# Kernel optimization log

Measured on AMD Instinct MI355X. Metric: run time of the kernel, lower is better.

Reference implementation:

```python
import jax, jax.numpy as jnp
import numpy as np

N_NODES = 50000


def setup_inputs() -> dict:
    key = jax.random.key(0)
    ks = jax.random.split(key, 6)
    nfeat, nhid, hops, nedges = 256, 64, 4, 800000
    x = jax.random.normal(ks[0], (N_NODES, nfeat), dtype=jnp.float32)
    W = jax.random.normal(ks[1], (hops, nfeat, nhid), dtype=jnp.float32) / np.sqrt(nfeat)
    b = jax.random.normal(ks[2], (hops, nhid), dtype=jnp.float32) * 0.01
    adj_rows = jax.random.randint(ks[3], (hops, nedges), 0, N_NODES, dtype=jnp.int32)
    adj_cols = jax.random.randint(ks[4], (hops, nedges), 0, N_NODES, dtype=jnp.int32)
    # normalize-ish positive edge weights, as in a GCN-normalized adjacency
    adj_vals = jax.random.uniform(ks[5], (hops, nedges), dtype=jnp.float32) / 16.0
    return {"x": x, "W": W, "b": b, "adj_rows": adj_rows,
            "adj_cols": adj_cols, "adj_vals": adj_vals}


def reference(x, W, b, adj_rows, adj_cols, adj_vals):
    # SIGN forward (eval mode: dropout = identity).
    # For each hop i: h = x @ W[i] + b[i]; out_i = spmm(adj_i, h)
    # spmm in COO form: out[r] = sum_{e: rows[e]==r} vals[e] * h[cols[e]]
    n = x.shape[0]
    hops = W.shape[0]
    outs = []
    for i in range(hops):  # small fixed hop count (layers+1)
        h = x @ W[i] + b[i]                      # [N, nhid] dense GEMM
        msgs = adj_vals[i][:, None] * h[adj_cols[i]]  # [E, nhid] gather
        outs.append(jax.ops.segment_sum(msgs, adj_rows[i], num_segments=n))
    return jax.nn.elu(jnp.concatenate(outs, axis=1))  # [N, hops*nhid]
```

## Files before the change

### kernel.cpp

```cpp
#include <hip/hip_runtime.h>
#include <hip/hip_bf16.h>
#include <math.h>

#define N_NODES 50000
#define NFEAT 256
#define NHID 64
#define HOPS 4
#define NEDGES 800000
#define NBINS (HOPS * N_NODES)

#define BROWS 256
#define NBUCK 196
#define NBK_ALL (HOPS * NBUCK)
#define CHUNK 8192
#define NCHUNK ((NEDGES + CHUNK - 1) / CHUNK)
#define FS_CAP 8192

#define GM 64
#define LDP 40
#define NGBLK ((N_NODES + GM - 1) / GM)

typedef short bf16x8 __attribute__((ext_vector_type(8)));
typedef float f32x4 __attribute__((ext_vector_type(4)));

static __device__ __forceinline__ unsigned short f2bf(float f) {
    __hip_bfloat16 h = __float2bfloat16(f);
    return *reinterpret_cast<unsigned short*>(&h);
}

__global__ __launch_bounds__(256) void castx_kernel(const float* __restrict__ x,
                                                    unsigned short* __restrict__ Xbf) {
    const int i = blockIdx.x * 256 + threadIdx.x;
    const size_t base = (size_t)i * 8;
    if (base < (size_t)N_NODES * NFEAT) {
        const float4 a = *(const float4*)&x[base];
        const float4 c = *(const float4*)&x[base + 4];
        unsigned short o[8] = {f2bf(a.x), f2bf(a.y), f2bf(a.z), f2bf(a.w),
                               f2bf(c.x), f2bf(c.y), f2bf(c.z), f2bf(c.w)};
        *(bf16x8*)&Xbf[base] = *(const bf16x8*)o;
    }
}

__global__ __launch_bounds__(256) void castw_kernel(const float* __restrict__ W,
                                                    unsigned short* __restrict__ Wt) {
    const int idx = blockIdx.x * 256 + threadIdx.x;
    if (idx < HOPS * NFEAT * NHID) {
        const int hop = idx >> 14;
        const int k = (idx >> 6) & 255;
        const int c = idx & 63;
        Wt[((size_t)(hop * 64 + c)) * NFEAT + k] = f2bf(W[idx]);
    }
}

__global__ __launch_bounds__(256) void gemm_bf_kernel(const unsigned short* __restrict__ Xbf,
                                                      const unsigned short* __restrict__ Wt,
                                                      const float* __restrict__ b,
                                                      __hip_bfloat16* __restrict__ H) {
    __shared__ unsigned short A_lds[GM * LDP];
    __shared__ unsigned short B_lds[256 * LDP];

    const int t = threadIdx.x;
    const int lane = t & 63;
    const int w = t >> 6;
    const int quad = lane >> 4;
    const int m16 = lane & 15;
    const int row0 = blockIdx.x * GM;

    f32x4 acc[4][4];
#pragma unroll
    for (int mt = 0; mt < 4; ++mt)
#pragma unroll
        for (int nt = 0; nt < 4; ++nt) acc[mt][nt] = (f32x4){0.f, 0.f, 0.f, 0.f};

    for (int ks = 0; ks < 8; ++ks) {
        const int k0 = ks * 32;
        {
            const int r = t >> 2;
            const int kq = (t & 3) * 8;
            bf16x8 v = {0, 0, 0, 0, 0, 0, 0, 0};
            if (row0 + r < N_NODES)
                v = *(const bf16x8*)&Xbf[(size_t)(row0 + r) * NFEAT + k0 + kq];
            *(bf16x8*)&A_lds[r * LDP + kq] = v;
        }
#pragma unroll
        for (int q = 0; q < 4; ++q) {
            const int kq = q * 8;
            const bf16x8 v = *(const bf16x8*)&Wt[(size_t)t * NFEAT + k0 + kq];
            *(bf16x8*)&B_lds[t * LDP + kq] = v;
        }
        __syncthreads();

        bf16x8 af[4], bf[4];
#pragma unroll
        for (int mt = 0; mt < 4; ++mt)
            af[mt] = *(const bf16x8*)&A_lds[(mt * 16 + m16) * LDP + quad * 8];
#pragma unroll
        for (int nt = 0; nt < 4; ++nt)
            bf[nt] = *(const bf16x8*)&B_lds[(w * 64 + nt * 16 + m16) * LDP + quad * 8];
#pragma unroll
        for (int mt = 0; mt < 4; ++mt)
#pragma unroll
            for (int nt = 0; nt < 4; ++nt)
                acc[mt][nt] = __builtin_amdgcn_mfma_f32_16x16x32_bf16(
                    af[mt], bf[nt], acc[mt][nt], 0, 0, 0);
        __syncthreads();
    }

#pragma unroll
    for (int nt = 0; nt < 4; ++nt) {
        const int col = w * 64 + nt * 16 + m16;
        const float bias = b[col];
#pragma unroll
        for (int mt = 0; mt < 4; ++mt) {
#pragma unroll
            for (int r = 0; r < 4; ++r) {
                const int row = row0 + mt * 16 + quad * 4 + r;
                if (row < N_NODES)
                    H[(size_t)row * 256 + col] = __float2bfloat16(acc[mt][nt][r] + bias);
            }
        }
    }
}

__global__ __launch_bounds__(256) void gemm_mfma_kernel(const float* __restrict__ x,
                                                        const float* __restrict__ W,
                                                        const float* __restrict__ b,
                                                        __hip_bfloat16* __restrict__ H) {
    __shared__ unsigned short A_lds[GM * LDP];
    __shared__ unsigned short B_lds[256 * LDP];

    const int t = threadIdx.x;
    const int lane = t & 63;
    const int w = t >> 6;
    const int quad = lane >> 4;
    const int m16 = lane & 15;
    const int row0 = blockIdx.x * GM;

    f32x4 acc[4][4];
#pragma unroll
    for (int mt = 0; mt < 4; ++mt)
#pragma unroll
        for (int nt = 0; nt < 4; ++nt) acc[mt][nt] = (f32x4){0.f, 0.f, 0.f, 0.f};

    for (int ks = 0; ks < 8; ++ks) {
        const int k0 = ks * 32;
#pragma unroll
        for (int it = 0; it < 2; ++it) {
            const int i = t + it * 256;
            const int r = i >> 3;
            const int kq = (i & 7) * 4;
            float4 v = make_float4(0.f, 0.f, 0.f, 0.f);
            if (row0 + r < N_NODES)
                v = *(const float4*)&x[(size_t)(row0 + r) * NFEAT + k0 + kq];
            unsigned short* d = &A_lds[r * LDP + kq];
            d[0] = f2bf(v.x); d[1] = f2bf(v.y); d[2] = f2bf(v.z); d[3] = f2bf(v.w);
        }
#pragma unroll
        for (int it = 0; it < 8; ++it) {
            const int i = t + it * 256;
            const int n4 = i & 63;
            const int kk = i >> 6;
            const int hop = n4 >> 4;
            const int j = (n4 & 15) * 4;
            const float4 v = *(const float4*)&W[(size_t)hop * (NFEAT * NHID)
                                                + (size_t)(k0 + kk) * NHID + j];
            B_lds[(n4 * 4 + 0) * LDP + kk] = f2bf(v.x);
            B_lds[(n4 * 4 + 1) * LDP + kk] = f2bf(v.y);
            B_lds[(n4 * 4 + 2) * LDP + kk] = f2bf(v.z);
            B_lds[(n4 * 4 + 3) * LDP + kk] = f2bf(v.w);
        }
        __syncthreads();

        bf16x8 af[4], bf[4];
#pragma unroll
        for (int mt = 0; mt < 4; ++mt)
            af[mt] = *(const bf16x8*)&A_lds[(mt * 16 + m16) * LDP + quad * 8];
#pragma unroll
        for (int nt = 0; nt < 4; ++nt)
            bf[nt] = *(const bf16x8*)&B_lds[(w * 64 + nt * 16 + m16) * LDP + quad * 8];
#pragma unroll
        for (int mt = 0; mt < 4; ++mt)
#pragma unroll
            for (int nt = 0; nt < 4; ++nt)
                acc[mt][nt] = __builtin_amdgcn_mfma_f32_16x16x32_bf16(
                    af[mt], bf[nt], acc[mt][nt], 0, 0, 0);
        __syncthreads();
    }

#pragma unroll
    for (int nt = 0; nt < 4; ++nt) {
        const int col = w * 64 + nt * 16 + m16;
        const float bias = b[col];
#pragma unroll
        for (int mt = 0; mt < 4; ++mt) {
#pragma unroll
            for (int r = 0; r < 4; ++r) {
                const int row = row0 + mt * 16 + quad * 4 + r;
                if (row < N_NODES)
                    H[(size_t)row * 256 + col] = __float2bfloat16(acc[mt][nt][r] + bias);
            }
        }
    }
}

__global__ __launch_bounds__(256) void bhist_kernel(const int* __restrict__ rows,
                                                    int* __restrict__ bucket_cnt) {
    __shared__ int h[NBUCK];
    const int t = threadIdx.x;
    for (int i = t; i < NBUCK; i += 256) h[i] = 0;
    __syncthreads();
    const int hop = blockIdx.y;
    const int e0 = blockIdx.x * CHUNK;
    const int n = min(CHUNK, NEDGES - e0);
    const size_t base = (size_t)hop * NEDGES + e0;
    for (int i = t; i < n; i += 256) {
        atomicAdd(&h[rows[base + i] >> 8], 1);
    }
    __syncthreads();
    for (int i = t; i < NBUCK; i += 256) {
        if (h[i]) atomicAdd(&bucket_cnt[hop * NBUCK + i], h[i]);
    }
}

__global__ __launch_bounds__(256) void bscan_kernel(const int* __restrict__ cnt,
                                                    int* __restrict__ start,
                                                    int* __restrict__ cursor,
                                                    int* __restrict__ offsets) {
    __shared__ int s[256];
    const int t = threadIdx.x;
    int v[4];
    int tsum = 0;
#pragma unroll
    for (int i = 0; i < 4; ++i) {
        const int idx = t * 4 + i;
        v[i] = (idx < NBK_ALL) ? cnt[idx] : 0;
        tsum += v[i];
    }
    s[t] = tsum;
    __syncthreads();
    for (int off = 1; off < 256; off <<= 1) {
        const int a = (t >= off) ? s[t - off] : 0;
        __syncthreads();
        s[t] += a;
        __syncthreads();
    }
    int run = s[t] - tsum;
#pragma unroll
    for (int i = 0; i < 4; ++i) {
        const int idx = t * 4 + i;
        if (idx < NBK_ALL) {
            start[idx] = run;
            cursor[idx] = run;
            run += v[i];
        }
    }
    if (t == 255) {
        start[NBK_ALL] = run;
        offsets[NBINS] = run;
    }
}

__global__ __launch_bounds__(256) void partition_kernel(const int* __restrict__ rows,
                                                        const int* __restrict__ cols,
                                                        const float* __restrict__ vals,
                                                        int* __restrict__ cursor,
                                                        int2* __restrict__ partbuf) {
    __shared__ int2 pay[CHUNK];
    __shared__ int h[NBUCK], excl[NBUCK], gbase[NBUCK], lcur[NBUCK];
    __shared__ int s[256];
    const int t = threadIdx.x;
    const int hop = blockIdx.y;
    const int e0 = blockIdx.x * CHUNK;
    const int n = min(CHUNK, NEDGES - e0);
    const size_t base = (size_t)hop * NEDGES + e0;

    for (int i = t; i < NBUCK; i += 256) h[i] = 0;
    __syncthreads();

    int myrow[CHUNK / 256];
#pragma unroll
    for (int j = 0; j < CHUNK / 256; ++j) {
        const int i = t + j * 256;
        if (i < n) {
            const int r = rows[base + i];
            myrow[j] = r;
            atomicAdd(&h[r >> 8], 1);
        }
    }
    __syncthreads();

    const int hv = (t < NBUCK) ? h[t] : 0;
    s[t] = hv;
    __syncthreads();
    for (int off = 1; off < 256; off <<= 1) {
        const int a = (t >= off) ? s[t - off] : 0;
        __syncthreads();
        s[t] += a;
        __syncthreads();
    }
    if (t < NBUCK) {
        const int ex = s[t] - hv;
        excl[t] = ex;
        lcur[t] = ex;
        gbase[t] = hv ? atomicAdd(&cursor[hop * NBUCK + t], hv) : 0;
    }
    __syncthreads();

#pragma unroll
    for (int j = 0; j < CHUNK / 256; ++j) {
        const int i = t + j * 256;
        if (i < n) {
            const int r = myrow[j];
            const int c = cols[base + i];
            const float v = vals[base + i];
            const int pos = atomicAdd(&lcur[r >> 8], 1);
            pay[pos] = make_int2((r << 16) | c, __float_as_int(v));
        }
    }
    __syncthreads();

    for (int i = t; i < n; i += 256) {
        const int2 p = pay[i];
        const int bk = ((unsigned)p.x) >> 24;
        partbuf[gbase[bk] + (i - excl[bk])] = p;
    }
}

__global__ __launch_bounds__(256) void fsort_kernel(const int* __restrict__ start,
                                                    int2* __restrict__ partbuf,
                                                    int* __restrict__ offsets) {
    __shared__ int2 pay[FS_CAP];
    __shared__ int h[BROWS], excl[BROWS], cur[BROWS];
    __shared__ int s[256];
    const int t = threadIdx.x;
    const int hop = blockIdx.y;
    const int bucket = blockIdx.x;
    const int g = hop * NBUCK + bucket;
    const int s0 = start[g];
    const int n = min(start[g + 1] - s0, FS_CAP);

    h[t] = 0;
    __syncthreads();

    for (int i = t; i < n; i += 256) {
        const int2 p = partbuf[s0 + i];
        pay[i] = p;
        atomicAdd(&h[((unsigned)p.x >> 16) & 255], 1);
    }
    __syncthreads();

    const int hv = h[t];
    s[t] = hv;
    __syncthreads();
    for (int off = 1; off < 256; off <<= 1) {
        const int a = (t >= off) ? s[t - off] : 0;
        __syncthreads();
        s[t] += a;
        __syncthreads();
    }
    const int ex = s[t] - hv;
    excl[t] = ex;
    cur[t] = 0;
    const int row = bucket * BROWS + t;
    if (row < N_NODES) offsets[hop * N_NODES + row] = s0 + ex;
    __syncthreads();

    for (int i = t; i < n; i += 256) {
        const int2 p = pay[i];
        const int rl = ((unsigned)p.x >> 16) & 255;
        const int pos = s0 + excl[rl] + atomicAdd(&cur[rl], 1);
        partbuf[pos] = make_int2(p.x & 0xFFFF, p.y);
    }
}

__global__ __launch_bounds__(256) void csr_gather_kernel(const __hip_bfloat16* __restrict__ H,
                                                         const int* __restrict__ offsets,
                                                         const int2* __restrict__ epk,
                                                         float* __restrict__ out) {
    const int t = threadIdx.x;
    const int f = t & 63;
    const int w = t >> 6;
    const int hop = blockIdx.y;
    const int row0w = blockIdx.x * 64 + w * 16;
    if (row0w >= N_NODES) return;
    const int bin0 = hop * N_NODES + row0w;

    int off_l = 0;
    if (f <= 16) off_l = offsets[bin0 + f];

    const unsigned short* Hf = (const unsigned short*)H + hop * 64 + f;
    float* outp = out + (size_t)row0w * 256 + hop * 64 + f;

    for (int r = 0; r < 16; ++r) {
        const int s  = __builtin_amdgcn_readlane(off_l, r);
        const int e2 = __builtin_amdgcn_readlane(off_l, r + 1);
        float acc = 0.f;
        int e = s;
        for (; e + 8 <= e2; e += 8) {
            const int2 m = epk[e + (f & 7)];
            float h8[8];
#pragma unroll
            for (int j = 0; j < 8; ++j) {
                const int col = __builtin_amdgcn_readlane(m.x, j);
                h8[j] = __uint_as_float((unsigned)Hf[(size_t)col << 8] << 16);
            }
#pragma unroll
            for (int j = 0; j < 8; ++j) {
                const float val = __uint_as_float((unsigned)__builtin_amdgcn_readlane(m.y, j));
                acc = fmaf(val, h8[j], acc);
            }
        }
        if (e < e2) {
            const int2 m = epk[e + (f & 7)];
            const int rem = e2 - e;
            for (int j = 0; j < rem; ++j) {
                const int col = __builtin_amdgcn_readlane(m.x, j);
                const float val = __uint_as_float((unsigned)__builtin_amdgcn_readlane(m.y, j));
                acc = fmaf(val, __uint_as_float((unsigned)Hf[(size_t)col << 8] << 16), acc);
            }
        }
        acc = acc > 0.f ? acc : expf(acc) - 1.f;
        outp[(size_t)r * 256] = acc;
    }
}

#define EPW 8
__global__ __launch_bounds__(256) void scatter_kernel(const __hip_bfloat16* __restrict__ H,
                                                      const int* __restrict__ rows,
                                                      const int* __restrict__ cols,
                                                      const float* __restrict__ vals,
                                                      float* __restrict__ out) {
    const int lane = threadIdx.x & 63;
    const int wid = __builtin_amdgcn_readfirstlane(threadIdx.x >> 6);
    const int hop = blockIdx.y;
    const int e0 = (blockIdx.x * 4 + wid) * EPW;
    const int base = hop * NEDGES;
    const int hoff = hop * 64 + lane;
#pragma unroll
    for (int i = 0; i < EPW; ++i) {
        const int e = e0 + i;
        const int r = rows[base + e];
        const int c = cols[base + e];
        const float v = vals[base + e];
        unsafeAtomicAdd(&out[(size_t)r * 256 + hoff],
                        v * __bfloat162float(H[(size_t)c * 256 + hoff]));
    }
}

__global__ __launch_bounds__(256) void elu_kernel(float* __restrict__ out, int n4) {
    const int i = blockIdx.x * 256 + threadIdx.x;
    if (i < n4) {
        float4 v = ((float4*)out)[i];
        v.x = v.x > 0.f ? v.x : expf(v.x) - 1.f;
        v.y = v.y > 0.f ? v.y : expf(v.y) - 1.f;
        v.z = v.z > 0.f ? v.z : expf(v.z) - 1.f;
        v.w = v.w > 0.f ? v.w : expf(v.w) - 1.f;
        ((float4*)out)[i] = v;
    }
}

extern "C" void kernel_launch(void* const* d_in, const int* in_sizes, int n_in,
                              void* d_out, int out_size, void* d_ws, size_t ws_size,
                              hipStream_t stream) {
    const float* x        = (const float*)d_in[0];
    const float* W        = (const float*)d_in[1];
    const float* b        = (const float*)d_in[2];
    const int*   adj_rows = (const int*)d_in[3];
    const int*   adj_cols = (const int*)d_in[4];
    const float* adj_vals = (const float*)d_in[5];
    float* out = (float*)d_out;

    char* w = (char*)d_ws;
    size_t off = 0;
    __hip_bfloat16* H = (__hip_bfloat16*)(w + off);
    off += (size_t)N_NODES * 256 * 2;
    int2*  partbuf    = (int2*)(w + off);  off += (size_t)HOPS * NEDGES * 8;
    int*   offsets    = (int*)(w + off);   off += (((size_t)(NBINS + 1)) * 4 + 255) & ~255ull;
    int*   bucket_cnt = (int*)(w + off);   off += ((size_t)NBK_ALL * 4 + 255) & ~255ull;
    int*   bstart     = (int*)(w + off);   off += (((size_t)NBK_ALL + 1) * 4 + 255) & ~255ull;
    int*   bcursor    = (int*)(w + off);   off += ((size_t)NBK_ALL * 4 + 255) & ~255ull;
    const bool use_sorted = (ws_size >= off);

    unsigned short* Xbf = (unsigned short*)partbuf;
    unsigned short* Wt  = (unsigned short*)offsets;

    if (use_sorted) {
        castx_kernel<<<(N_NODES * NFEAT / 8 + 255) / 256, 256, 0, stream>>>(x, Xbf);
        castw_kernel<<<(HOPS * NFEAT * NHID + 255) / 256, 256, 0, stream>>>(W, Wt);
        gemm_bf_kernel<<<NGBLK, 256, 0, stream>>>(Xbf, Wt, b, H);

        hipMemsetAsync(bucket_cnt, 0, (size_t)NBK_ALL * 4, stream);
        bhist_kernel<<<dim3(NCHUNK, HOPS), 256, 0, stream>>>(adj_rows, bucket_cnt);
        bscan_kernel<<<1, 256, 0, stream>>>(bucket_cnt, bstart, bcursor, offsets);
        partition_kernel<<<dim3(NCHUNK, HOPS), 256, 0, stream>>>(adj_rows, adj_cols,
                                                                 adj_vals, bcursor, partbuf);
        fsort_kernel<<<dim3(NBUCK, HOPS), 256, 0, stream>>>(bstart, partbuf, offsets);
        csr_gather_kernel<<<dim3((N_NODES + 63) / 64, HOPS), 256, 0, stream>>>(
            H, offsets, partbuf, out);
    } else {
        gemm_mfma_kernel<<<NGBLK, 256, 0, stream>>>(x, W, b, H);
        hipMemsetAsync(d_out, 0, (size_t)out_size * sizeof(float), stream);
        scatter_kernel<<<dim3(NEDGES / (4 * EPW), HOPS), 256, 0, stream>>>(
            H, adj_rows, adj_cols, adj_vals, out);
        elu_kernel<<<(out_size / 4 + 255) / 256, 256, 0, stream>>>(out, out_size / 4);
    }
}
```

Baseline: 361.5 us.

## Shrink sort buckets to 64 rows and stage per-wave edge metadata in LDS

```diff
diff --git a/kernel.cpp b/kernel.cpp
--- a/kernel.cpp
+++ b/kernel.cpp
@@ -9,12 +9,13 @@
 #define NEDGES 800000
 #define NBINS (HOPS * N_NODES)
 
-#define BROWS 256
-#define NBUCK 196
+#define BROWS 64
+#define NBUCK 782
 #define NBK_ALL (HOPS * NBUCK)
-#define CHUNK 8192
+#define CHUNK 4096
 #define NCHUNK ((NEDGES + CHUNK - 1) / CHUNK)
-#define FS_CAP 8192
+#define FS_CAP 2048
+#define MCAP 512
 
 #define GM 64
 #define LDP 40
@@ -214,7 +215,7 @@
     const int n = min(CHUNK, NEDGES - e0);
     const size_t base = (size_t)hop * NEDGES + e0;
     for (int i = t; i < n; i += 256) {
-        atomicAdd(&h[rows[base + i] >> 8], 1);
+        atomicAdd(&h[rows[base + i] >> 6], 1);
     }
     __syncthreads();
     for (int i = t; i < NBUCK; i += 256) {
@@ -222,17 +223,18 @@
     }
 }
 
+#define SCAN_V ((NBK_ALL + 255) / 256)
 __global__ __launch_bounds__(256) void bscan_kernel(const int* __restrict__ cnt,
                                                     int* __restrict__ start,
                                                     int* __restrict__ cursor,
                                                     int* __restrict__ offsets) {
     __shared__ int s[256];
     const int t = threadIdx.x;
-    int v[4];
+    int v[SCAN_V];
     int tsum = 0;
 #pragma unroll
-    for (int i = 0; i < 4; ++i) {
-        const int idx = t * 4 + i;
+    for (int i = 0; i < SCAN_V; ++i) {
+        const int idx = t * SCAN_V + i;
         v[i] = (idx < NBK_ALL) ? cnt[idx] : 0;
         tsum += v[i];
     }
@@ -246,8 +248,8 @@
     }
     int run = s[t] - tsum;
 #pragma unroll
-    for (int i = 0; i < 4; ++i) {
-        const int idx = t * 4 + i;
+    for (int i = 0; i < SCAN_V; ++i) {
+        const int idx = t * SCAN_V + i;
         if (idx < NBK_ALL) {
             start[idx] = run;
             cursor[idx] = run;
@@ -284,13 +286,20 @@
         if (i < n) {
             const int r = rows[base + i];
             myrow[j] = r;
-            atomicAdd(&h[r >> 8], 1);
-        }
-    }
-    __syncthreads();
-
-    const int hv = (t < NBUCK) ? h[t] : 0;
-    s[t] = hv;
+            atomicAdd(&h[r >> 6], 1);
+        }
+    }
+    __syncthreads();
+
+    int pv[4];
+    int tsum = 0;
+#pragma unroll
+    for (int i = 0; i < 4; ++i) {
+        const int idx = t * 4 + i;
+        pv[i] = (idx < NBUCK) ? h[idx] : 0;
+        tsum += pv[i];
+    }
+    s[t] = tsum;
     __syncthreads();
     for (int off = 1; off < 256; off <<= 1) {
         const int a = (t >= off) ? s[t - off] : 0;
@@ -298,11 +307,16 @@
         s[t] += a;
         __syncthreads();
     }
-    if (t < NBUCK) {
-        const int ex = s[t] - hv;
-        excl[t] = ex;
-        lcur[t] = ex;
-        gbase[t] = hv ? atomicAdd(&cursor[hop * NBUCK + t], hv) : 0;
+    int run = s[t] - tsum;
+#pragma unroll
+    for (int i = 0; i < 4; ++i) {
+        const int idx = t * 4 + i;
+        if (idx < NBUCK) {
+            excl[idx] = run;
+            lcur[idx] = run;
+            gbase[idx] = pv[i] ? atomicAdd(&cursor[hop * NBUCK + idx], pv[i]) : 0;
+            run += pv[i];
+        }
     }
     __syncthreads();
 
@@ -313,7 +327,7 @@
             const int r = myrow[j];
             const int c = cols[base + i];
             const float v = vals[base + i];
-            const int pos = atomicAdd(&lcur[r >> 8], 1);
+            const int pos = atomicAdd(&lcur[r >> 6], 1);
             pay[pos] = make_int2((r << 16) | c, __float_as_int(v));
         }
     }
@@ -321,7 +335,7 @@
 
     for (int i = t; i < n; i += 256) {
         const int2 p = pay[i];
-        const int bk = ((unsigned)p.x) >> 24;
+        const int bk = ((unsigned)p.x) >> 22;
         partbuf[gbase[bk] + (i - excl[bk])] = p;
     }
 }
@@ -339,17 +353,17 @@
     const int s0 = start[g];
     const int n = min(start[g + 1] - s0, FS_CAP);
 
-    h[t] = 0;
+    if (t < BROWS) h[t] = 0;
     __syncthreads();
 
     for (int i = t; i < n; i += 256) {
         const int2 p = partbuf[s0 + i];
         pay[i] = p;
-        atomicAdd(&h[((unsigned)p.x >> 16) & 255], 1);
-    }
-    __syncthreads();
-
-    const int hv = h[t];
+        atomicAdd(&h[((unsigned)p.x >> 16) & (BROWS - 1)], 1);
+    }
+    __syncthreads();
+
+    const int hv = (t < BROWS) ? h[t] : 0;
     s[t] = hv;
     __syncthreads();
     for (int off = 1; off < 256; off <<= 1) {
@@ -358,16 +372,18 @@
         s[t] += a;
         __syncthreads();
     }
-    const int ex = s[t] - hv;
-    excl[t] = ex;
-    cur[t] = 0;
-    const int row = bucket * BROWS + t;
-    if (row < N_NODES) offsets[hop * N_NODES + row] = s0 + ex;
+    if (t < BROWS) {
+        const int ex = s[t] - hv;
+        excl[t] = ex;
+        cur[t] = 0;
+        const int row = bucket * BROWS + t;
+        if (row < N_NODES) offsets[hop * N_NODES + row] = s0 + ex;
+    }
     __syncthreads();
 
     for (int i = t; i < n; i += 256) {
         const int2 p = pay[i];
-        const int rl = ((unsigned)p.x >> 16) & 255;
+        const int rl = ((unsigned)p.x >> 16) & (BROWS - 1);
         const int pos = s0 + excl[rl] + atomicAdd(&cur[rl], 1);
         partbuf[pos] = make_int2(p.x & 0xFFFF, p.y);
     }
@@ -377,6 +393,7 @@
                                                          const int* __restrict__ offsets,
                                                          const int2* __restrict__ epk,
                                                          float* __restrict__ out) {
+    __shared__ int2 meta[4][MCAP + 8];
     const int t = threadIdx.x;
     const int f = t & 63;
     const int w = t >> 6;
@@ -387,40 +404,75 @@
 
     int off_l = 0;
     if (f <= 16) off_l = offsets[bin0 + f];
+    const int s0w = __builtin_amdgcn_readlane(off_l, 0);
+    const int s1w = __builtin_amdgcn_readlane(off_l, 16);
+    const int cnt = s1w - s0w;
 
     const unsigned short* Hf = (const unsigned short*)H + hop * 64 + f;
     float* outp = out + (size_t)row0w * 256 + hop * 64 + f;
 
-    for (int r = 0; r < 16; ++r) {
-        const int s  = __builtin_amdgcn_readlane(off_l, r);
-        const int e2 = __builtin_amdgcn_readlane(off_l, r + 1);
-        float acc = 0.f;
-        int e = s;
-        for (; e + 8 <= e2; e += 8) {
-            const int2 m = epk[e + (f & 7)];
-            float h8[8];
-#pragma unroll
-            for (int j = 0; j < 8; ++j) {
-                const int col = __builtin_amdgcn_readlane(m.x, j);
-                h8[j] = __uint_as_float((unsigned)Hf[(size_t)col << 8] << 16);
+    if (cnt <= MCAP) {
+        int2* M = meta[w];
+        for (int i = f; i < cnt; i += 64) M[i] = epk[s0w + i];
+        if (f < 8) M[cnt + f] = make_int2(0, 0);
+
+        for (int r = 0; r < 16; ++r) {
+            const int s  = __builtin_amdgcn_readlane(off_l, r) - s0w;
+            const int e2 = __builtin_amdgcn_readlane(off_l, r + 1) - s0w;
+            float acc = 0.f;
+            for (int g = s; g < e2; g += 8) {
+                int2 mm[8];
+#pragma unroll
+                for (int j = 0; j < 8; ++j) mm[j] = M[g + j];
+                float h8[8];
+#pragma unroll
+                for (int j = 0; j < 8; ++j)
+                    h8[j] = __uint_as_float(
+                        (unsigned)Hf[(size_t)(unsigned)mm[j].x << 8] << 16);
+#pragma unroll
+                for (int j = 0; j < 8; ++j) {
+                    const float vj = (g + j < e2) ? __int_as_float(mm[j].y) : 0.f;
+                    acc = fmaf(vj, h8[j], acc);
+                }
             }
-#pragma unroll
-            for (int j = 0; j < 8; ++j) {
-                const float val = __uint_as_float((unsigned)__builtin_amdgcn_readlane(m.y, j));
-                acc = fmaf(val, h8[j], acc);
+            acc = acc > 0.f ? acc : expf(acc) - 1.f;
+            outp[(size_t)r * 256] = acc;
+        }
+    } else {
+        for (int r = 0; r < 16; ++r) {
+            const int s  = __builtin_amdgcn_readlane(off_l, r);
+            const int e2 = __builtin_amdgcn_readlane(off_l, r + 1);
+            float acc = 0.f;
+            int e = s;
+            for (; e + 8 <= e2; e += 8) {
+                const int2 m = epk[e + (f & 7)];
+                float h8[8];
+#pragma unroll
+                for (int j = 0; j < 8; ++j) {
+                    const int col = __builtin_amdgcn_readlane(m.x, j);
+                    h8[j] = __uint_as_float((unsigned)Hf[(size_t)col << 8] << 16);
+                }
+#pragma unroll
+                for (int j = 0; j < 8; ++j) {
+                    const float val =
+                        __uint_as_float((unsigned)__builtin_amdgcn_readlane(m.y, j));
+                    acc = fmaf(val, h8[j], acc);
+                }
             }
-        }
-        if (e < e2) {
-            const int2 m = epk[e + (f & 7)];
-            const int rem = e2 - e;
-            for (int j = 0; j < rem; ++j) {
-                const int col = __builtin_amdgcn_readlane(m.x, j);
-                const float val = __uint_as_float((unsigned)__builtin_amdgcn_readlane(m.y, j));
-                acc = fmaf(val, __uint_as_float((unsigned)Hf[(size_t)col << 8] << 16), acc);
+            if (e < e2) {
+                const int2 m = epk[e + (f & 7)];
+                const int rem = e2 - e;
+                for (int j = 0; j < rem; ++j) {
+                    const int col = __builtin_amdgcn_readlane(m.x, j);
+                    const float val =
+                        __uint_as_float((unsigned)__builtin_amdgcn_readlane(m.y, j));
+                    acc = fmaf(val, __uint_as_float((unsigned)Hf[(size_t)col << 8] << 16),
+                               acc);
+                }
             }
-        }
-        acc = acc > 0.f ? acc : expf(acc) - 1.f;
-        outp[(size_t)r * 256] = acc;
+            acc = acc > 0.f ? acc : expf(acc) - 1.f;
+            outp[(size_t)r * 256] = acc;
+        }
     }
 }
 
```

After: 336.6 us. -6.9%, faster.
